# Kernel tuning notes

Measured on AMD Instinct MI355X. Metric: run time of the kernel, lower is better.

## Reference

```python
import math
import jax, jax.numpy as jnp
import numpy as np
from jax.scipy.special import xlogy, gammaln

WINDOW = 256  # window_size from init_kwargs


def get_positional_embed(seq_len, feature_size):
    # Enformer-style relative positional features; feature_size % 6 == 0.
    distances = jnp.arange(-seq_len + 1, seq_len, dtype=jnp.float32)  # (2W-1,)
    nb = feature_size // 6
    absd = jnp.abs(distances)[:, None]  # (2W-1, 1)
    # exponential basis
    max_range = math.log(seq_len) / math.log(2.0)
    half_life = 2.0 ** jnp.linspace(3.0, max_range, nb)
    feat_exp = jnp.exp(-math.log(2.0) / half_life[None, :] * absd)
    # central mask basis
    center_widths = 2.0 ** jnp.arange(1, nb + 1, dtype=jnp.float32) - 1.0
    feat_cm = (center_widths[None, :] > absd).astype(jnp.float32)
    # gamma pdf basis
    stddev = seq_len / (2.0 * nb)
    start_mean = seq_len / nb
    mean = jnp.linspace(start_mean, float(seq_len), nb)[None, :]
    concentration = (mean / stddev) ** 2
    rate = mean / stddev ** 2
    log_unnorm = xlogy(concentration - 1.0, absd) - rate * absd
    log_norm = gammaln(concentration) - concentration * jnp.log(rate)
    prob = jnp.exp(log_unnorm - log_norm) + 1e-8
    feat_gamma = prob / jnp.max(prob, axis=-1, keepdims=True)
    emb = jnp.concatenate([feat_exp, feat_cm, feat_gamma], axis=-1)
    return jnp.concatenate([emb, jnp.sign(distances)[:, None] * emb], axis=-1)  # (2W-1, F)


def relative_shift_swin(x):
    # x: (b, h, nw, t1, t2) with t2 = 2*t1 - 1  ->  (b, h, nw, t1, t1)
    b, h, w, t1, t2 = x.shape
    x = jnp.pad(x, ((0, 0), (0, 0), (0, 0), (0, 0), (1, 0)))  # pad zero at front of last dim
    x = x.reshape(b, h, w, t2 + 1, t1)
    x = x[:, :, :, 1:, :].reshape(b, h, w, t1, t2)
    return x[..., :(t2 + 1) // 2]


def setup_inputs() -> dict:
    key = jax.random.key(0)
    ks = jax.random.split(key, 7)
    B, N, C, H, D = 2, 8192, 768, 12, 64
    return {
        "x": jax.random.normal(ks[0], (B, N, C), jnp.float32),
        "w_qkv": jax.random.normal(ks[1], (C, 3 * H * D), jnp.float32) * 0.02,
        "w_out": jax.random.normal(ks[2], (H * D, C), jnp.float32) * 0.02,
        "b_out": jnp.zeros((C,), jnp.float32),
        "w_rel": jax.random.normal(ks[3], (C, H * D), jnp.float32) * 0.02,
        "rel_content_bias": jax.random.normal(ks[4], (1, H, 1, 1, D), jnp.float32),
        "rel_pos_bias": jax.random.normal(ks[5], (1, H, 1, 1, D), jnp.float32),
    }


def reference(x, w_qkv, w_out, b_out, w_rel, rel_content_bias, rel_pos_bias):
    b, n, c = x.shape
    H, D = rel_content_bias.shape[1], rel_content_bias.shape[-1]
    W = WINDOW
    nw = n // W  # n divisible by W (no padding branch)
    # qkv projection; output layout of to_qkv is (h, d, k) per 'b n (h d k) -> k b h n d'
    qkv = (x @ w_qkv).reshape(b, n, H, D, 3)
    q = jnp.transpose(qkv[..., 0], (0, 2, 1, 3)).reshape(b, H, nw, W, D)
    k = jnp.transpose(qkv[..., 1], (0, 2, 1, 3)).reshape(b, H, nw, W, D)
    v = jnp.transpose(qkv[..., 2], (0, 2, 1, 3)).reshape(b, H, nw, W, D)
    # relative position keys: 'n (h d) -> h n d'
    F = w_rel.shape[0]
    positions = get_positional_embed(W, F)  # (2W-1, F)
    rel_k = jnp.transpose((positions @ w_rel).reshape(2 * W - 1, H, D), (1, 0, 2))  # (H, 2W-1, D)
    # content attention (scaled); position attention (unscaled, as in source)
    content_attn = jnp.einsum('bhwid,bhwjd->bhwij', q + rel_content_bias, k) * (D ** -0.5)
    rel_logits = jnp.einsum('bhwid,hjd->bhwij', q + rel_pos_bias, rel_k)  # (b,H,nw,W,2W-1)
    position_attn = relative_shift_swin(rel_logits)  # (b,H,nw,W,W)
    attn = jax.nn.softmax(content_attn + position_attn, axis=-1)
    out = jnp.einsum('bhwij,bhwjd->bhwid', attn, v)  # (b,H,nw,W,D)
    out = jnp.transpose(out, (0, 2, 3, 1, 4)).reshape(b, nw, W, H * D)  # 'b h w n d -> b w n (h d)'
    out = out @ w_out + b_out
    return out.reshape(b, n, c)
```

## Files before the change

### kernel.cpp

```cpp
#include <hip/hip_runtime.h>
#include <math.h>

typedef __attribute__((ext_vector_type(8))) short bf8;
typedef __attribute__((ext_vector_type(4))) float f4;
typedef __attribute__((ext_vector_type(2))) unsigned u2;
typedef __attribute__((ext_vector_type(4))) unsigned u4;

__device__ __forceinline__ float bf2f(short s) {
    union { unsigned u; float f; } v; v.u = ((unsigned)(unsigned short)s) << 16; return v.f;
}
__device__ __forceinline__ short f2bf(float f) {
    return (short)((__float_as_uint(f) + 0x8000u) >> 16);
}
__device__ __forceinline__ unsigned pk2(float a, float b) {
    unsigned ua = __float_as_uint(a) + 0x8000u;
    unsigned ub = __float_as_uint(b) + 0x8000u;
    return __builtin_amdgcn_perm(ub, ua, 0x07060302u);
}
__device__ __forceinline__ void gload16(const short* g, short* l) {
    __builtin_amdgcn_global_load_lds(
        (const __attribute__((address_space(1))) void*)g,
        (__attribute__((address_space(3))) void*)l,
        16, 0, 0);
}

__global__ __launch_bounds__(256) void xb_k(const float* __restrict__ X, short* __restrict__ XB) {
    long idx = (long)blockIdx.x * 256 + threadIdx.x;
    const float* src = X + idx * 8;
    float4 v0 = *(const float4*)(src);
    float4 v1 = *(const float4*)(src + 4);
    u4 p; p.x = pk2(v0.x, v0.y); p.y = pk2(v0.z, v0.w);
    p.z = pk2(v1.x, v1.y); p.w = pk2(v1.z, v1.w);
    *(u4*)(XB + idx * 8) = p;
}

__global__ void pos_kernel(short* __restrict__ P) {
    const int row = blockIdx.x;
    const int j = threadIdx.x;
    if (row == 511) {
        for (int t = j; t < 768; t += 128) P[511 * 768 + t] = 0;
        return;
    }
    const double dist = (double)(row - 255);
    const double ad = fabs(dist);
    double hl = exp2(3.0 + 5.0 * (double)j / 127.0);
    double fe = exp(-M_LN2 / hl * ad);
    double cw = exp2((double)(j + 1)) - 1.0;
    double fc = (cw > ad) ? 1.0 : 0.0;
    double m = 2.0 + 2.0 * (double)j;
    double conc = m * m;
    double lun = (ad == 0.0) ? -INFINITY : (conc - 1.0) * log(ad);
    lun -= m * ad;
    double lnorm = lgamma(conc) - conc * log(m);
    double prob = exp(lun - lnorm) + 1e-8;
    __shared__ double red[128];
    red[j] = prob;
    __syncthreads();
    for (int s2 = 64; s2 > 0; s2 >>= 1) {
        if (j < s2) red[j] = fmax(red[j], red[j + s2]);
        __syncthreads();
    }
    double fg = prob / red[0];
    float sg = (dist > 0.0) ? 1.f : ((dist < 0.0) ? -1.f : 0.f);
    int base = row * 768;
    P[base + j]        = f2bf((float)fe);
    P[base + 128 + j]  = f2bf((float)fc);
    P[base + 256 + j]  = f2bf((float)fg);
    P[base + 384 + j]  = f2bf(sg * (float)fe);
    P[base + 512 + j]  = f2bf(sg * (float)fc);
    P[base + 640 + j]  = f2bf(sg * (float)fg);
}

__global__ void wT_k(const float* __restrict__ W, short* __restrict__ WT,
                     int K, int N, int qperm) {
    int idx = blockIdx.x * 256 + threadIdx.x;
    int kq = K >> 2;
    if (idx >= N * kq) return;
    int n = idx / kq, k = (idx % kq) << 2;
    int rp = n;
    if (qperm) { int sel = n % 3, hd = n / 3; rp = sel * 768 + hd; }
    float a = W[(long)(k + 0) * N + n];
    float b = W[(long)(k + 1) * N + n];
    float c = W[(long)(k + 2) * N + n];
    float d = W[(long)(k + 3) * N + n];
    u2 r; r.x = pk2(a, b); r.y = pk2(c, d);
    *(u2*)(WT + (long)rp * K + k) = r;
}

__global__ __launch_bounds__(256) void gemm_k(
    const short* __restrict__ A, const short* __restrict__ BT,
    int M, int N, int K, int mode,
    short* __restrict__ Cb, float* __restrict__ Cf, const float* __restrict__ bias,
    short* __restrict__ Qo, short* __restrict__ Ko, short* __restrict__ Vt)
{
    __shared__ __attribute__((aligned(16))) short lds[2][8192];
    const int tid = threadIdx.x;
    const int lane = tid & 63;
    const int wave = tid >> 6;
    const int wm = wave >> 1, wn = wave & 1;
    const int c = lane & 15, quad = lane >> 4;
    const int m0 = blockIdx.x * 128, n0 = blockIdx.y * 128;
    const int lrow = lane >> 2;
    const int lslot = lane & 3;

    f4 acc[4][4];
#pragma unroll
    for (int i = 0; i < 4; ++i)
#pragma unroll
        for (int jx = 0; jx < 4; ++jx) acc[i][jx] = (f4){0.f, 0.f, 0.f, 0.f};

    const int nT = K >> 5;

    auto stage = [&](int buf, int k0) {
        short* As = &lds[buf][0];
        short* Bs = &lds[buf][4096];
#pragma unroll
        for (int i = 0; i < 2; ++i) {
            int grp = wave * 2 + i;
            int row = grp * 16 + lrow;
            int ss = lslot ^ ((row >> 1) & 3);
            const short* srcA;
            if (mode == 2) {
                int m = m0 + row;
                srcA = A + (((long)((m >> 13) * 12 + (k0 >> 6)) * 8192 + (m & 8191)) * 64
                            + (k0 & 63) + ss * 8);
            } else {
                srcA = A + (long)(m0 + row) * K + k0 + ss * 8;
            }
            gload16(srcA, &As[grp * 512]);
            const short* srcB = BT + (long)(n0 + row) * K + k0 + ss * 8;
            gload16(srcB, &Bs[grp * 512]);
        }
    };

    stage(0, 0);
    __syncthreads();

    for (int t = 0, cur = 0; t < nT; ++t, cur ^= 1) {
        if (t + 1 < nT) stage(cur ^ 1, (t + 1) << 5);
        const short* As = &lds[cur][0];
        const short* Bs = &lds[cur][4096];
        bf8 a[4], b[4];
#pragma unroll
        for (int mt = 0; mt < 4; ++mt) {
            int row = wm * 64 + mt * 16 + c;
            int slot = quad ^ ((row >> 1) & 3);
            a[mt] = *(const bf8*)(&As[row * 32 + slot * 8]);
        }
#pragma unroll
        for (int nt = 0; nt < 4; ++nt) {
            int row = wn * 64 + nt * 16 + c;
            int slot = quad ^ ((row >> 1) & 3);
            b[nt] = *(const bf8*)(&Bs[row * 32 + slot * 8]);
        }
#pragma unroll
        for (int mt = 0; mt < 4; ++mt)
#pragma unroll
            for (int nt = 0; nt < 4; ++nt)
                acc[mt][nt] = __builtin_amdgcn_mfma_f32_16x16x32_bf16(a[mt], b[nt], acc[mt][nt], 0, 0, 0);
        __syncthreads();
    }

    if (mode == 1) {
        const int sel = n0 / 768;
        if (sel == 2) {
#pragma unroll
            for (int mt = 0; mt < 4; ++mt)
#pragma unroll
                for (int nt = 0; nt < 4; ++nt)
#pragma unroll
                    for (int r = 0; r < 4; ++r) {
                        int m = m0 + wm * 64 + mt * 16 + quad * 4 + r;
                        int np = n0 - 1536 + wn * 64 + nt * 16 + c;
                        int h = np >> 6, d = np & 63;
                        int bb = m >> 13, nn = m & 8191;
                        long off = ((long)((bb * 12 + h) * 32 + (nn >> 8))) * 16384 + d * 256 + (nn & 255);
                        Vt[off] = f2bf(acc[mt][nt][r]);
                    }
        } else {
            short* dst = (sel == 0) ? Qo : Ko;
            const int nb = n0 - sel * 768;
#pragma unroll
            for (int mt = 0; mt < 4; ++mt)
#pragma unroll
                for (int nt = 0; nt < 4; ++nt)
#pragma unroll
                    for (int r = 0; r < 4; ++r) {
                        int m = m0 + wm * 64 + mt * 16 + quad * 4 + r;
                        int np = nb + wn * 64 + nt * 16 + c;
                        int h = np >> 6, d = np & 63;
                        int bb = m >> 13, nn = m & 8191;
                        long off = ((long)((bb * 12 + h) * 8192 + nn)) * 64 + d;
                        dst[off] = f2bf(acc[mt][nt][r]);
                    }
        }
    } else {
#pragma unroll
        for (int mt = 0; mt < 4; ++mt)
#pragma unroll
            for (int nt = 0; nt < 4; ++nt)
#pragma unroll
                for (int r = 0; r < 4; ++r) {
                    int m = m0 + wm * 64 + mt * 16 + quad * 4 + r;
                    int n = n0 + wn * 64 + nt * 16 + c;
                    float val = acc[mt][nt][r];
                    if (mode == 2) {
                        Cf[(long)m * N + n] = val + bias[n];
                    } else {
                        Cb[(long)m * N + n] = f2bf(val);
                    }
                }
    }
}

__global__ __launch_bounds__(256) void attn_k(
    short* __restrict__ Q, const short* __restrict__ Kk, const short* __restrict__ Vt,
    const short* __restrict__ RK,
    const float* __restrict__ rcb, const float* __restrict__ rpb)
{
    __shared__ __attribute__((aligned(16))) short Ks[256 * 64];
    __shared__ __attribute__((aligned(16))) short Ps[4][16 * 136];
    const int bid = blockIdx.x;
    const int low = bid & 7;
    const int wlo = low >> 1;
    const int hlo = low & 1;
    const int rest = bid >> 3;
    const int strip = rest & 3;
    const int t_ = rest >> 2;
    const int whi = t_ & 7;
    const int u_ = t_ >> 3;
    const int h = ((u_ % 6) << 1) | hlo;
    const int b = u_ / 6;
    const int w = (whi << 2) | wlo;
    const int tid = threadIdx.x, lane = tid & 63, wave = tid >> 6;
    const int c = lane & 15, quad = lane >> 4;
    const int i0w = strip * 64 + wave * 16;

    const long base_bh = ((long)(b * 12 + h) * 8192 + (long)w * 256) * 64;
    short* Qh = Q + base_bh;
    const short* Kh = Kk + base_bh;
    const short* Vw = Vt + (((long)(b * 12 + h) * 32 + w) << 14);
    const short* RKh = RK + h * 64;

#pragma unroll
    for (int i = 0; i < 8; ++i) {
        int p = tid + i * 256;
        int row = p >> 3, ls = p & 7;
        gload16(Kh + row * 64 + (ls ^ (row & 7)) * 8, &Ks[(wave * 64 + i * 256) * 8]);
    }

    bf8 qc[2], qp[2];
#pragma unroll
    for (int ks = 0; ks < 2; ++ks) {
        bf8 qraw = *(const bf8*)(Qh + (i0w + c) * 64 + ks * 32 + quad * 8);
        float4 cb0 = *(const float4*)(rcb + h * 64 + ks * 32 + quad * 8);
        float4 cb1 = *(const float4*)(rcb + h * 64 + ks * 32 + quad * 8 + 4);
        float4 pb0 = *(const float4*)(rpb + h * 64 + ks * 32 + quad * 8);
        float4 pb1 = *(const float4*)(rpb + h * 64 + ks * 32 + quad * 8 + 4);
        float cbv[8] = {cb0.x, cb0.y, cb0.z, cb0.w, cb1.x, cb1.y, cb1.z, cb1.w};
        float pbv[8] = {pb0.x, pb0.y, pb0.z, pb0.w, pb1.x, pb1.y, pb1.z, pb1.w};
#pragma unroll
        for (int u = 0; u < 8; ++u) {
            float qv = bf2f(qraw[u]);
            qc[ks][u] = f2bf(qv + cbv[u]);
            qp[ks][u] = f2bf(qv + pbv[u]);
        }
    }

    const int r0 = 240 - i0w;
    bf8 rfb[2][2];
#pragma unroll
    for (int t = 0; t < 2; ++t)
#pragma unroll
        for (int ks = 0; ks < 2; ++ks)
            rfb[t][ks] = *(const bf8*)(RKh + (long)(r0 + t * 16 + c) * 768 + ks * 32 + quad * 8);

    __syncthreads();

    f4 S[16], R[17];
#pragma unroll
    for (int ct = 0; ct < 16; ++ct) S[ct] = (f4){0.f, 0.f, 0.f, 0.f};
#pragma unroll
    for (int rt = 0; rt < 17; ++rt) R[rt] = (f4){0.f, 0.f, 0.f, 0.f};
#pragma unroll
    for (int t = 0; t < 17; ++t) {
        bf8 cur0 = rfb[t & 1][0], cur1 = rfb[t & 1][1];
        if (t + 2 < 17) {
#pragma unroll
            for (int ks = 0; ks < 2; ++ks)
                rfb[t & 1][ks] = *(const bf8*)(RKh + (long)(r0 + (t + 2) * 16 + c) * 768 + ks * 32 + quad * 8);
        }
        if (t < 16) {
            int row = t * 16 + c;
#pragma unroll
            for (int ks = 0; ks < 2; ++ks) {
                bf8 kf = *(const bf8*)(&Ks[row * 64 + (((ks * 4 + quad) ^ (row & 7))) * 8]);
                S[t] = __builtin_amdgcn_mfma_f32_16x16x32_bf16(qc[ks], kf, S[t], 0, 0, 0);
            }
        }
        R[t] = __builtin_amdgcn_mfma_f32_16x16x32_bf16(qp[0], cur0, R[t], 0, 0, 0);
        R[t] = __builtin_amdgcn_mfma_f32_16x16x32_bf16(qp[1], cur1, R[t], 0, 0, 0);
    }
    __syncthreads();

    short* Vs = Ks;
#pragma unroll
    for (int i = 0; i < 8; ++i) {
        int p = tid + i * 256;
        int row = p >> 5, ls = p & 31;
        gload16(Vw + row * 256 + (ls ^ ((row & 7) << 2)) * 8, &Vs[(wave * 2 + i * 8) * 256]);
    }

#pragma unroll
    for (int ct = 0; ct < 16; ++ct)
#pragma unroll
        for (int r = 0; r < 4; ++r) {
            int ip = quad * 4 + r;
            int src = (lane & 48) | ((15 - ip + c) & 15);
            float vA = __shfl(R[ct][r], src);
            float vB = __shfl(R[ct + 1][r], src);
            float pos = (c <= ip) ? vA : vB;
            S[ct][r] = S[ct][r] * 0.125f + pos;
        }

    float mx[4] = {-3.4e38f, -3.4e38f, -3.4e38f, -3.4e38f};
#pragma unroll
    for (int ct = 0; ct < 16; ++ct)
#pragma unroll
        for (int r = 0; r < 4; ++r) mx[r] = fmaxf(mx[r], S[ct][r]);
#pragma unroll
    for (int r = 0; r < 4; ++r)
#pragma unroll
        for (int o = 1; o < 16; o <<= 1) mx[r] = fmaxf(mx[r], __shfl_xor(mx[r], o));
    float sm[4] = {0.f, 0.f, 0.f, 0.f};
#pragma unroll
    for (int ct = 0; ct < 16; ++ct)
#pragma unroll
        for (int r = 0; r < 4; ++r) {
            float p = __expf(S[ct][r] - mx[r]);
            S[ct][r] = p;
            sm[r] += p;
        }
#pragma unroll
    for (int r = 0; r < 4; ++r)
#pragma unroll
        for (int o = 1; o < 16; o <<= 1) sm[r] += __shfl_xor(sm[r], o);
    float inv[4];
#pragma unroll
    for (int r = 0; r < 4; ++r) inv[r] = 1.0f / sm[r];

    __syncthreads();

    f4 O[4];
#pragma unroll
    for (int vt = 0; vt < 4; ++vt) O[vt] = (f4){0.f, 0.f, 0.f, 0.f};
#pragma unroll
    for (int half = 0; half < 2; ++half) {
#pragma unroll
        for (int ct = 0; ct < 8; ++ct)
#pragma unroll
            for (int r = 0; r < 4; ++r)
                Ps[wave][(quad * 4 + r) * 136 + ct * 16 + c] = f2bf(S[half * 8 + ct][r] * inv[r]);
#pragma unroll
        for (int kt = 0; kt < 4; ++kt) {
            bf8 af = *(const bf8*)(&Ps[wave][c * 136 + kt * 32 + quad * 8]);
#pragma unroll
            for (int vt = 0; vt < 4; ++vt) {
                int row = vt * 16 + c;
                int slot = (((half * 4 + kt) * 4 + quad) ^ ((row & 7) << 2));
                bf8 bv = *(const bf8*)(&Vs[row * 256 + slot * 8]);
                O[vt] = __builtin_amdgcn_mfma_f32_16x16x32_bf16(af, bv, O[vt], 0, 0, 0);
            }
        }
    }
#pragma unroll
    for (int vt = 0; vt < 4; ++vt)
#pragma unroll
        for (int r = 0; r < 4; ++r)
            Qh[(i0w + quad * 4 + r) * 64 + vt * 16 + c] = f2bf(O[vt][r]);
}

extern "C" void kernel_launch(void* const* d_in, const int* in_sizes, int n_in,
                              void* d_out, int out_size, void* d_ws, size_t ws_size,
                              hipStream_t stream) {
    const float* x     = (const float*)d_in[0];
    const float* w_qkv = (const float*)d_in[1];
    const float* w_out = (const float*)d_in[2];
    const float* b_out = (const float*)d_in[3];
    const float* w_rel = (const float*)d_in[4];
    const float* rcb   = (const float*)d_in[5];
    const float* rpb   = (const float*)d_in[6];

    char* ws = (char*)d_ws;
    short* wqkvT = (short*)(ws);
    short* woutT = (short*)(ws + 3538944L);
    short* wrelT = (short*)(ws + 4718592L);
    short* pos   = (short*)(ws + 5898240L);
    short* relk  = (short*)(ws + 6684672L);
    short* q     = (short*)(ws + 7471104L);
    short* k     = (short*)(ws + 32636928L);
    short* vT    = (short*)(ws + 57802752L);
    short* xb    = (short*)d_out;

    wT_k<<<(2304 * 192 + 255) / 256, 256, 0, stream>>>(w_qkv, wqkvT, 768, 2304, 1);
    wT_k<<<(768 * 192 + 255) / 256, 256, 0, stream>>>(w_out, woutT, 768, 768, 0);
    wT_k<<<(768 * 192 + 255) / 256, 256, 0, stream>>>(w_rel, wrelT, 768, 768, 0);
    pos_kernel<<<512, 128, 0, stream>>>(pos);
    xb_k<<<6144, 256, 0, stream>>>(x, xb);
    gemm_k<<<dim3(4, 6), 256, 0, stream>>>(pos, wrelT, 512, 768, 768, 0,
                                           relk, nullptr, nullptr, nullptr, nullptr, nullptr);
    gemm_k<<<dim3(128, 18), 256, 0, stream>>>(xb, wqkvT, 16384, 2304, 768, 1,
                                              nullptr, nullptr, nullptr, q, k, vT);
    attn_k<<<3072, 256, 0, stream>>>(q, k, vT, relk, rcb, rpb);
    gemm_k<<<dim3(128, 6), 256, 0, stream>>>(q, woutT, 16384, 768, 768, 2,
                                             nullptr, (float*)d_out, b_out, nullptr, nullptr, nullptr);
}
```

Measured before the change: 340.4 us.

## Stream relative-position logits per tile to cut registers and raise occupancy

Instead of computing all 17 relative-position logit tiles into a register array up front, each tile is now computed on the fly after the content scores and folded into the scores using a rolling previous/current rotated value. The P staging buffer shrinks to a 16x32 tile per wave, written and consumed one k-step at a time. A min-blocks-per-CU hint of 4 is added. Together these aim to lower VGPR and LDS pressure so more waves fit per CU. In exchange, the RK loads are no longer prefetched ahead of use and the per-k-step LDS round trip adds more synchronisation points within each wave.

```diff
diff --git a/kernel.cpp b/kernel.cpp
--- a/kernel.cpp
+++ b/kernel.cpp
@@ -213,13 +213,13 @@
     }
 }
 
-__global__ __launch_bounds__(256) void attn_k(
+__global__ __launch_bounds__(256, 4) void attn_k(
     short* __restrict__ Q, const short* __restrict__ Kk, const short* __restrict__ Vt,
     const short* __restrict__ RK,
     const float* __restrict__ rcb, const float* __restrict__ rpb)
 {
     __shared__ __attribute__((aligned(16))) short Ks[256 * 64];
-    __shared__ __attribute__((aligned(16))) short Ps[4][16 * 136];
+    __shared__ __attribute__((aligned(16))) short Ps[4][16 * 36];
     const int bid = blockIdx.x;
     const int low = bid & 7;
     const int wlo = low >> 1;
@@ -266,40 +266,19 @@
             qp[ks][u] = f2bf(qv + pbv[u]);
         }
     }
-
-    const int r0 = 240 - i0w;
-    bf8 rfb[2][2];
-#pragma unroll
-    for (int t = 0; t < 2; ++t)
-#pragma unroll
-        for (int ks = 0; ks < 2; ++ks)
-            rfb[t][ks] = *(const bf8*)(RKh + (long)(r0 + t * 16 + c) * 768 + ks * 32 + quad * 8);
-
     __syncthreads();
 
-    f4 S[16], R[17];
+    f4 S[16];
 #pragma unroll
     for (int ct = 0; ct < 16; ++ct) S[ct] = (f4){0.f, 0.f, 0.f, 0.f};
 #pragma unroll
-    for (int rt = 0; rt < 17; ++rt) R[rt] = (f4){0.f, 0.f, 0.f, 0.f};
-#pragma unroll
-    for (int t = 0; t < 17; ++t) {
-        bf8 cur0 = rfb[t & 1][0], cur1 = rfb[t & 1][1];
-        if (t + 2 < 17) {
-#pragma unroll
-            for (int ks = 0; ks < 2; ++ks)
-                rfb[t & 1][ks] = *(const bf8*)(RKh + (long)(r0 + (t + 2) * 16 + c) * 768 + ks * 32 + quad * 8);
-        }
-        if (t < 16) {
-            int row = t * 16 + c;
-#pragma unroll
-            for (int ks = 0; ks < 2; ++ks) {
-                bf8 kf = *(const bf8*)(&Ks[row * 64 + (((ks * 4 + quad) ^ (row & 7))) * 8]);
-                S[t] = __builtin_amdgcn_mfma_f32_16x16x32_bf16(qc[ks], kf, S[t], 0, 0, 0);
-            }
-        }
-        R[t] = __builtin_amdgcn_mfma_f32_16x16x32_bf16(qp[0], cur0, R[t], 0, 0, 0);
-        R[t] = __builtin_amdgcn_mfma_f32_16x16x32_bf16(qp[1], cur1, R[t], 0, 0, 0);
+    for (int t = 0; t < 16; ++t) {
+        int row = t * 16 + c;
+#pragma unroll
+        for (int ks = 0; ks < 2; ++ks) {
+            bf8 kf = *(const bf8*)(&Ks[row * 64 + (((ks * 4 + quad) ^ (row & 7))) * 8]);
+            S[t] = __builtin_amdgcn_mfma_f32_16x16x32_bf16(qc[ks], kf, S[t], 0, 0, 0);
+        }
     }
     __syncthreads();
 
@@ -311,17 +290,34 @@
         gload16(Vw + row * 256 + (ls ^ ((row & 7) << 2)) * 8, &Vs[(wave * 2 + i * 8) * 256]);
     }
 
-#pragma unroll
-    for (int ct = 0; ct < 16; ++ct)
-#pragma unroll
-        for (int r = 0; r < 4; ++r) {
-            int ip = quad * 4 + r;
-            int src = (lane & 48) | ((15 - ip + c) & 15);
-            float vA = __shfl(R[ct][r], src);
-            float vB = __shfl(R[ct + 1][r], src);
-            float pos = (c <= ip) ? vA : vB;
-            S[ct][r] = S[ct][r] * 0.125f + pos;
-        }
+    const int r0 = 240 - i0w;
+    int src_[4];
+#pragma unroll
+    for (int r = 0; r < 4; ++r) {
+        int ip = quad * 4 + r;
+        src_[r] = (lane & 48) | ((15 - ip + c) & 15);
+    }
+    float rotp[4], rotc[4];
+#pragma unroll
+    for (int t = 0; t < 17; ++t) {
+        bf8 rf0 = *(const bf8*)(RKh + (long)(r0 + t * 16 + c) * 768 + quad * 8);
+        bf8 rf1 = *(const bf8*)(RKh + (long)(r0 + t * 16 + c) * 768 + 32 + quad * 8);
+        f4 Rt = (f4){0.f, 0.f, 0.f, 0.f};
+        Rt = __builtin_amdgcn_mfma_f32_16x16x32_bf16(qp[0], rf0, Rt, 0, 0, 0);
+        Rt = __builtin_amdgcn_mfma_f32_16x16x32_bf16(qp[1], rf1, Rt, 0, 0, 0);
+#pragma unroll
+        for (int r = 0; r < 4; ++r) rotc[r] = __shfl(Rt[r], src_[r]);
+        if (t > 0) {
+#pragma unroll
+            for (int r = 0; r < 4; ++r) {
+                int ip = quad * 4 + r;
+                float pos = (c <= ip) ? rotp[r] : rotc[r];
+                S[t - 1][r] = S[t - 1][r] * 0.125f + pos;
+            }
+        }
+#pragma unroll
+        for (int r = 0; r < 4; ++r) rotp[r] = rotc[r];
+    }
 
     float mx[4] = {-3.4e38f, -3.4e38f, -3.4e38f, -3.4e38f};
 #pragma unroll
@@ -355,22 +351,19 @@
 #pragma unroll
     for (int vt = 0; vt < 4; ++vt) O[vt] = (f4){0.f, 0.f, 0.f, 0.f};
 #pragma unroll
-    for (int half = 0; half < 2; ++half) {
-#pragma unroll
-        for (int ct = 0; ct < 8; ++ct)
-#pragma unroll
-            for (int r = 0; r < 4; ++r)
-                Ps[wave][(quad * 4 + r) * 136 + ct * 16 + c] = f2bf(S[half * 8 + ct][r] * inv[r]);
-#pragma unroll
-        for (int kt = 0; kt < 4; ++kt) {
-            bf8 af = *(const bf8*)(&Ps[wave][c * 136 + kt * 32 + quad * 8]);
-#pragma unroll
-            for (int vt = 0; vt < 4; ++vt) {
-                int row = vt * 16 + c;
-                int slot = (((half * 4 + kt) * 4 + quad) ^ ((row & 7) << 2));
-                bf8 bv = *(const bf8*)(&Vs[row * 256 + slot * 8]);
-                O[vt] = __builtin_amdgcn_mfma_f32_16x16x32_bf16(af, bv, O[vt], 0, 0, 0);
-            }
+    for (int kt = 0; kt < 8; ++kt) {
+#pragma unroll
+        for (int r = 0; r < 4; ++r) {
+            Ps[wave][(quad * 4 + r) * 36 + c]      = f2bf(S[kt * 2][r] * inv[r]);
+            Ps[wave][(quad * 4 + r) * 36 + 16 + c] = f2bf(S[kt * 2 + 1][r] * inv[r]);
+        }
+        bf8 af = *(const bf8*)(&Ps[wave][c * 36 + quad * 8]);
+#pragma unroll
+        for (int vt = 0; vt < 4; ++vt) {
+            int row = vt * 16 + c;
+            int slot = ((kt * 4 + quad) ^ ((row & 7) << 2));
+            bf8 bv = *(const bf8*)(&Vs[row * 256 + slot * 8]);
+            O[vt] = __builtin_amdgcn_mfma_f32_16x16x32_bf16(af, bv, O[vt], 0, 0, 0);
         }
     }
 #pragma unroll
```

Result: slower. 350.8 us (+3.1%).
